# Optimization experiments

Hardware: AMD Instinct MI355X
Metric: run time of the kernel (lower is better)

Reference implementation:

```python
import jax, jax.numpy as jnp
import numpy as np

# UKF constants (Merwe scaled sigma points)
ALPHA, BETA, KAPPA = 1.0, 2.0, 0.0
JITTER = 1e-4
S_DIM, C_DIM, M_DIM, H_DIM = 8, 2, 4, 32


def setup_inputs() -> dict:
    B, T = 1024, 256
    key = jax.random.key(0)
    ks = jax.random.split(key, 11)
    inp = {
        "X0": 0.1 * jax.random.normal(ks[0], (B, S_DIM), dtype=jnp.float32),
        "u": jax.random.normal(ks[1], (B, T, C_DIM), dtype=jnp.float32),
        "y": jax.random.normal(ks[2], (B, T, M_DIM), dtype=jnp.float32),
        # learned process model f(x,u) = x + tanh([x;u] W1 + b1) W2 + b2
        "W1": 0.1 * jax.random.normal(ks[3], (S_DIM + C_DIM, H_DIM), dtype=jnp.float32),
        "b1": jnp.zeros((H_DIM,), dtype=jnp.float32),
        "W2": 0.1 * jax.random.normal(ks[4], (H_DIM, S_DIM), dtype=jnp.float32),
        "b2": jnp.zeros((S_DIM,), dtype=jnp.float32),
        # linear measurement model h(x) = Hm x
        "Hm": 0.3 * jax.random.normal(ks[5], (M_DIM, S_DIM), dtype=jnp.float32),
        # learned diagonal noise / initial covariance (softplus parameterized)
        "lq": -3.0 + 0.1 * jax.random.normal(ks[6], (S_DIM,), dtype=jnp.float32),
        "lr": -2.0 + 0.1 * jax.random.normal(ks[7], (M_DIM,), dtype=jnp.float32),
        "lp0": -1.0 + 0.1 * jax.random.normal(ks[8], (S_DIM,), dtype=jnp.float32),
    }
    return inp


def reference(X0, u, y, W1, b1, W2, b2, Hm, lq, lr, lp0):
    B, n = X0.shape
    T = u.shape[1]
    lam = ALPHA ** 2 * (n + KAPPA) - n
    c = n + lam
    Wm = jnp.concatenate([jnp.array([lam / c], dtype=X0.dtype),
                          jnp.full((2 * n,), 0.5 / c, dtype=X0.dtype)])
    Wc = Wm.at[0].add(1.0 - ALPHA ** 2 + BETA)
    I = jnp.eye(n, dtype=X0.dtype)

    Q = jnp.diag(jax.nn.softplus(lq))            # [n,n] process noise
    R = jnp.diag(jax.nn.softplus(lr))            # [m,m] measurement noise
    P0 = jnp.broadcast_to(jnp.diag(jax.nn.softplus(lp0)), (B, n, n))  # P0(X0)

    def f(pts, u_t):  # pts [B,2n+1,n], u_t [B,C]
        uu = jnp.broadcast_to(u_t[:, None, :], pts.shape[:2] + (u_t.shape[-1],))
        z = jnp.concatenate([pts, uu], axis=-1)
        return pts + jnp.tanh(z @ W1 + b1) @ W2 + b2

    def step(carry, inp_t):
        x, P = carry            # x [B,n], P [B,n,n]
        u_t, y_t = inp_t        # u at i-1, y at i
        # sigma points via Cholesky of scaled covariance
        L = jnp.linalg.cholesky(c * P + JITTER * I)
        offs = jnp.swapaxes(L, -1, -2)  # [B,n,n]: row i = i-th column of L
        pts = jnp.concatenate([x[:, None], x[:, None] + offs, x[:, None] - offs], axis=1)  # [B,2n+1,n]
        # predict
        pts_f = f(pts, u_t)
        x_pred = jnp.einsum('s,bsn->bn', Wm, pts_f)
        dx = pts_f - x_pred[:, None]
        P_pred = jnp.einsum('s,bsn,bsm->bnm', Wc, dx, dx) + Q
        P_pred = 0.5 * (P_pred + jnp.swapaxes(P_pred, -1, -2)) + JITTER * I
        # measurement update (linear h reused on propagated sigma points)
        y_pts = pts_f @ Hm.T
        y_pred = jnp.einsum('s,bsm->bm', Wm, y_pts)
        dy = y_pts - y_pred[:, None]
        Sy = jnp.einsum('s,bsi,bsj->bij', Wc, dy, dy) + R
        Sy = 0.5 * (Sy + jnp.swapaxes(Sy, -1, -2))
        Pxy = jnp.einsum('s,bsn,bsm->bnm', Wc, dx, dy)
        # K = Pxy Sy^{-1} via solve on Sy (SPD)
        K = jnp.swapaxes(jnp.linalg.solve(Sy, jnp.swapaxes(Pxy, -1, -2)), -1, -2)
        x_new = x_pred + jnp.einsum('bnm,bm->bn', K, y_t - y_pred)
        P_new = P_pred - K @ Sy @ jnp.swapaxes(K, -1, -2)
        P_new = 0.5 * (P_new + jnp.swapaxes(P_new, -1, -2)) + JITTER * I
        q_e = 0.5 * jnp.linalg.slogdet(P_pred)[1]  # [B]
        r_e = 0.5 * jnp.linalg.slogdet(Sy)[1]      # [B]
        return (x_new, P_new), (x_new, P_new, q_e, r_e)

    # steps i = 1..T-1 use u[:, i-1] and y[:, i]
    u_seq = jnp.swapaxes(u[:, :T - 1], 0, 1)  # [T-1,B,C]
    y_seq = jnp.swapaxes(y[:, 1:], 0, 1)      # [T-1,B,M]
    _, (Xs, Ps, qs, rs) = jax.lax.scan(step, (X0, P0), (u_seq, y_seq))

    X = jnp.concatenate([X0[:, None], jnp.swapaxes(Xs, 0, 1)], axis=1)        # [B,T,n]
    P = jnp.concatenate([P0[:, None], jnp.swapaxes(Ps, 0, 1)], axis=1)        # [B,T,n,n]
    zcol = jnp.zeros((X0.shape[0], 1), dtype=X0.dtype)
    q_entr = jnp.concatenate([zcol, jnp.swapaxes(qs, 0, 1)], axis=1)          # [B,T]
    r_entr = jnp.concatenate([zcol, jnp.swapaxes(rs, 0, 1)], axis=1)          # [B,T]
    return X, P, q_entr, r_entr
```

## Files before the change

### kernel.cpp

```cpp
#include <hip/hip_runtime.h>
#include <math.h>

#define B_LEN 1024
#define T_LEN 256
#define HST 36
#define TS 20

__device__ __forceinline__ float fast_rcp(float x) { return __builtin_amdgcn_rcpf(x); }
__device__ __forceinline__ float fast_rsq(float x) { return __builtin_amdgcn_rsqf(x); }
__device__ __forceinline__ float lane_bcast(float v, int l) {
    return __int_as_float(__builtin_amdgcn_readlane(__float_as_int(v), l));
}
__device__ __forceinline__ float fast_tanh(float x) {
    float e = __expf(2.0f * x);
    return 1.0f - 2.0f * fast_rcp(e + 1.0f);
}
__device__ __forceinline__ float softplus_f(float x) {
    return (x > 20.0f) ? x : log1pf(expf(x));
}
__device__ __forceinline__ float wdot17(const float* __restrict__ a,
                                        const float* __restrict__ b) {
    float full = 0.0f;
    #pragma unroll
    for (int c = 0; c < 4; ++c) {
        const float4 av = *(const float4*)&a[c * 4];
        const float4 bv = *(const float4*)&b[c * 4];
        full += av.x * bv.x + av.y * bv.y + av.z * bv.z + av.w * bv.w;
    }
    full += a[16] * b[16];
    return 0.0625f * full + 1.9375f * a[0] * b[0];
}

__global__ __launch_bounds__(128, 2)
void ukf_kernel(const float* __restrict__ X0, const float* __restrict__ U,
                const float* __restrict__ Y,  const float* __restrict__ W1,
                const float* __restrict__ B1, const float* __restrict__ W2,
                const float* __restrict__ B2, const float* __restrict__ HM,
                const float* __restrict__ LQ, const float* __restrict__ LR,
                const float* __restrict__ LP0, float* __restrict__ out)
{
    const int tid  = threadIdx.x;
    const int wid  = tid >> 6;
    const int lane = tid & 63;
    const int b    = blockIdx.x;
    const int k8   = lane & 7;
    const int g8   = lane >> 3;
    const int i8   = g8;
    const int j8   = k8;
    const int h32  = lane & 31;
    const int p2   = lane >> 5;
    const int m4   = lane & 3;
    const int sy   = lane >> 2;

    __shared__ __align__(16) float u_sh[T_LEN * 2];
    __shared__ __align__(16) float y_sh[T_LEN * 4];
    __shared__ __align__(16) float pts_sh[17 * 8];
    __shared__ __align__(16) float hid_sh[17 * HST];
    __shared__ __align__(16) float pf_sh[17 * 8];
    __shared__ __align__(16) float dxT_sh[8 * TS];
    __shared__ __align__(16) float ypT_sh[4 * TS];
    __shared__ __align__(16) float xp_sh[8];
    __shared__ __align__(16) float ypred_sh[4];
    __shared__ __align__(16) float Sy_sh[16];
    __shared__ __align__(16) float Si_sh[16];
    __shared__ __align__(16) float Pxy_sh[32];
    __shared__ __align__(16) float K_sh[32];
    __shared__ __align__(16) float Pp_sh[64];

    for (int k = tid; k < T_LEN * 2; k += 128) u_sh[k] = U[(size_t)b * (T_LEN * 2) + k];
    for (int k = tid; k < T_LEN * 4; k += 128) y_sh[k] = Y[(size_t)b * (T_LEN * 4) + k];

    float w1r[10];
    #pragma unroll
    for (int d = 0; d < 10; ++d) w1r[d] = W1[d * 32 + h32];
    const float b1r = B1[h32];
    float w2r[32];
    #pragma unroll
    for (int h = 0; h < 32; ++h) w2r[h] = W2[h * 8 + k8];
    const float b2r = B2[k8];
    float hmr[8];
    #pragma unroll
    for (int d = 0; d < 8; ++d) hmr[d] = HM[m4 * 8 + d];

    const float qdiag = softplus_f(LQ[i8]);
    const float rdiag = softplus_f(LR[m4]);

    const size_t Xbase = (size_t)b * T_LEN * 8;
    const size_t Pbase = (size_t)B_LEN * T_LEN * 8  + (size_t)b * T_LEN * 64;
    const size_t qbase = (size_t)B_LEN * T_LEN * 72 + (size_t)b * T_LEN;
    const size_t rbase = (size_t)B_LEN * T_LEN * 73 + (size_t)b * T_LEN;

    float xn[8], Pc[8];
    {
        const float4 xa = *(const float4*)&X0[b * 8];
        const float4 xb = *(const float4*)&X0[b * 8 + 4];
        xn[0] = xa.x; xn[1] = xa.y; xn[2] = xa.z; xn[3] = xa.w;
        xn[4] = xb.x; xn[5] = xb.y; xn[6] = xb.z; xn[7] = xb.w;
        const float p0k = softplus_f(LP0[k8]);
        #pragma unroll
        for (int i = 0; i < 8; ++i) Pc[i] = (i == k8) ? p0k : 0.0f;
    }
    if (wid == 0) {
        out[Pbase + lane] = Pc[g8];
        if (lane == 0) {
            *(float4*)&out[Xbase]     = make_float4(xn[0], xn[1], xn[2], xn[3]);
            *(float4*)&out[Xbase + 4] = make_float4(xn[4], xn[5], xn[6], xn[7]);
            out[qbase] = 0.0f; out[rbase] = 0.0f;
        }
    }

    for (int t = 1; t < T_LEN; ++t) {
        if (wid == 0) {
            float a[8];
            #pragma unroll
            for (int i = 0; i < 8; ++i) a[i] = 8.0f * Pc[i] + ((i == k8) ? 1e-4f : 0.0f);
            #pragma unroll
            for (int j = 0; j < 8; ++j) {
                const float dj  = lane_bcast(a[j], j);
                const float rv  = fast_rsq(dj);
                const float rv2 = rv * rv;
                float u[8];
                #pragma unroll
                for (int i = j + 1; i < 8; ++i) u[i] = lane_bcast(a[i], j);
                if (k8 == j) {
                    a[j] = dj * rv;
                    #pragma unroll
                    for (int i = j + 1; i < 8; ++i) a[i] *= rv;
                } else if (k8 > j) {
                    const float tt = a[j] * rv2;
                    #pragma unroll
                    for (int i = j + 1; i < 8; ++i) a[i] = fmaf(-tt, u[i], a[i]);
                }
            }
            float Lc[8];
            #pragma unroll
            for (int i = 0; i < 8; ++i) Lc[i] = (i >= k8) ? a[i] : 0.0f;
            if (g8 == 0) {
                *(float4*)&pts_sh[(1 + k8) * 8] =
                    make_float4(xn[0] + Lc[0], xn[1] + Lc[1], xn[2] + Lc[2], xn[3] + Lc[3]);
                *(float4*)&pts_sh[(1 + k8) * 8 + 4] =
                    make_float4(xn[4] + Lc[4], xn[5] + Lc[5], xn[6] + Lc[6], xn[7] + Lc[7]);
            } else if (g8 == 1) {
                *(float4*)&pts_sh[(9 + k8) * 8] =
                    make_float4(xn[0] - Lc[0], xn[1] - Lc[1], xn[2] - Lc[2], xn[3] - Lc[3]);
                *(float4*)&pts_sh[(9 + k8) * 8 + 4] =
                    make_float4(xn[4] - Lc[4], xn[5] - Lc[5], xn[6] - Lc[6], xn[7] - Lc[7]);
            } else if (g8 == 2 && k8 == 0) {
                *(float4*)&pts_sh[0] = make_float4(xn[0], xn[1], xn[2], xn[3]);
                *(float4*)&pts_sh[4] = make_float4(xn[4], xn[5], xn[6], xn[7]);
            }
        }
        __syncthreads();

        {
            const float u0 = u_sh[(t - 1) * 2 + 0];
            const float u1 = u_sh[(t - 1) * 2 + 1];
            const float ub = b1r + u0 * w1r[8] + u1 * w1r[9];
            if (wid == 0) {
                #pragma unroll
                for (int p = 0; p < 4; ++p) {
                    const int s = 2 * p + p2;
                    const float4 pa = *(const float4*)&pts_sh[s * 8];
                    const float4 pb = *(const float4*)&pts_sh[s * 8 + 4];
                    float acc = ub
                        + pa.x * w1r[0] + pa.y * w1r[1] + pa.z * w1r[2] + pa.w * w1r[3]
                        + pb.x * w1r[4] + pb.y * w1r[5] + pb.z * w1r[6] + pb.w * w1r[7];
                    hid_sh[s * HST + h32] = fast_tanh(acc);
                }
            } else {
                #pragma unroll
                for (int p = 0; p < 4; ++p) {
                    const int s = 8 + 2 * p + p2;
                    const float4 pa = *(const float4*)&pts_sh[s * 8];
                    const float4 pb = *(const float4*)&pts_sh[s * 8 + 4];
                    float acc = ub
                        + pa.x * w1r[0] + pa.y * w1r[1] + pa.z * w1r[2] + pa.w * w1r[3]
                        + pb.x * w1r[4] + pb.y * w1r[5] + pb.z * w1r[6] + pb.w * w1r[7];
                    hid_sh[s * HST + h32] = fast_tanh(acc);
                }
                if (p2 == 0) {
                    const float4 pa = *(const float4*)&pts_sh[16 * 8];
                    const float4 pb = *(const float4*)&pts_sh[16 * 8 + 4];
                    float acc = ub
                        + pa.x * w1r[0] + pa.y * w1r[1] + pa.z * w1r[2] + pa.w * w1r[3]
                        + pb.x * w1r[4] + pb.y * w1r[5] + pb.z * w1r[6] + pb.w * w1r[7];
                    hid_sh[16 * HST + h32] = fast_tanh(acc);
                }
            }
            const int srow = (wid == 0) ? g8 : (8 + g8);
            float acc = b2r;
            #pragma unroll
            for (int h = 0; h < 32; h += 4) {
                const float4 hv = *(const float4*)&hid_sh[srow * HST + h];
                acc += hv.x * w2r[h] + hv.y * w2r[h + 1] + hv.z * w2r[h + 2] + hv.w * w2r[h + 3];
            }
            pf_sh[srow * 8 + k8] = pts_sh[srow * 8 + k8] + acc;
            if (wid == 1 && lane < 8) {
                float a16 = b2r;
                #pragma unroll
                for (int h = 0; h < 32; h += 4) {
                    const float4 hv = *(const float4*)&hid_sh[16 * HST + h];
                    a16 += hv.x * w2r[h] + hv.y * w2r[h + 1] + hv.z * w2r[h + 2] + hv.w * w2r[h + 3];
                }
                pf_sh[16 * 8 + lane] = pts_sh[16 * 8 + lane] + a16;
            }
        }
        __syncthreads();

        if (wid == 0) {
            const float v0   = pf_sh[i8 * 8 + j8];
            const float v1   = pf_sh[(8 + i8) * 8 + j8];
            const float pf16 = (i8 == 0) ? pf_sh[16 * 8 + j8] : 0.0f;
            float part = ((i8 == 0) ? pf16 : v0) + v1;
            part += __shfl_xor(part, 8);
            part += __shfl_xor(part, 16);
            part += __shfl_xor(part, 32);
            const float xp = part * 0.0625f;
            if (i8 == 0) xp_sh[j8] = xp;
            dxT_sh[j8 * TS + i8]       = v0 - xp;
            dxT_sh[j8 * TS + 8 + i8]   = v1 - xp;
            if (i8 == 0) dxT_sh[j8 * TS + 16] = pf16 - xp;
        } else {
            float yv0, yv16 = 0.0f;
            {
                const float4 pa = *(const float4*)&pf_sh[sy * 8];
                const float4 pb = *(const float4*)&pf_sh[sy * 8 + 4];
                yv0 = pa.x * hmr[0] + pa.y * hmr[1] + pa.z * hmr[2] + pa.w * hmr[3]
                    + pb.x * hmr[4] + pb.y * hmr[5] + pb.z * hmr[6] + pb.w * hmr[7];
            }
            if (sy == 0) {
                const float4 pa = *(const float4*)&pf_sh[16 * 8];
                const float4 pb = *(const float4*)&pf_sh[16 * 8 + 4];
                yv16 = pa.x * hmr[0] + pa.y * hmr[1] + pa.z * hmr[2] + pa.w * hmr[3]
                     + pb.x * hmr[4] + pb.y * hmr[5] + pb.z * hmr[6] + pb.w * hmr[7];
            }
            float py = (sy == 0) ? yv16 : yv0;
            py += __shfl_xor(py, 4);
            py += __shfl_xor(py, 8);
            py += __shfl_xor(py, 16);
            py += __shfl_xor(py, 32);
            const float ypred = py * 0.0625f;
            if (lane < 4) ypred_sh[lane] = ypred;
            ypT_sh[m4 * TS + sy] = yv0 - ypred;
            if (sy == 0) ypT_sh[m4 * TS + 16] = yv16 - ypred;
        }
        __syncthreads();

        float Ppc[8];
        if (wid == 0) {
            const float Ppred = wdot17(&dxT_sh[i8 * TS], &dxT_sh[j8 * TS])
                              + ((i8 == j8) ? (qdiag + 1e-4f) : 0.0f);
            Pp_sh[lane] = Ppred;
            if (lane < 32) {
                const int ii = lane >> 2, mm = lane & 3;
                Pxy_sh[lane] = wdot17(&dxT_sh[ii * TS], &ypT_sh[mm * TS]);
            }
            #pragma unroll
            for (int i = 0; i < 8; ++i) Ppc[i] = Pp_sh[i * 8 + k8];
        } else {
            if (lane < 16)
                Sy_sh[lane] = wdot17(&ypT_sh[sy * TS], &ypT_sh[m4 * TS])
                            + ((sy == m4) ? rdiag : 0.0f);
            float s_[16];
            {
                const float4 r0v = *(const float4*)&Sy_sh[0];
                const float4 r1v = *(const float4*)&Sy_sh[4];
                const float4 r2v = *(const float4*)&Sy_sh[8];
                const float4 r3v = *(const float4*)&Sy_sh[12];
                s_[0]=r0v.x;  s_[1]=r0v.y;  s_[2]=r0v.z;  s_[3]=r0v.w;
                s_[4]=r1v.x;  s_[5]=r1v.y;  s_[6]=r1v.z;  s_[7]=r1v.w;
                s_[8]=r2v.x;  s_[9]=r2v.y;  s_[10]=r2v.z; s_[11]=r2v.w;
                s_[12]=r3v.x; s_[13]=r3v.y; s_[14]=r3v.z; s_[15]=r3v.w;
            }
            const float d0 = s_[0];
            const float r0 = fast_rsq(d0);
            const float L10 = s_[4] * r0, L20 = s_[8] * r0, L30 = s_[12] * r0;
            const float d1 = s_[5] - L10 * L10;
            const float r1 = fast_rsq(d1);
            const float L21 = (s_[9]  - L20 * L10) * r1;
            const float L31 = (s_[13] - L30 * L10) * r1;
            const float d2_ = s_[10] - L20 * L20 - L21 * L21;
            const float r2 = fast_rsq(d2_);
            const float L32 = (s_[14] - L30 * L20 - L31 * L21) * r2;
            const float d3 = s_[15] - L30 * L30 - L31 * L31 - L32 * L32;
            const float r3 = fast_rsq(d3);
            if (lane == 0)
                out[rbase + t] = 0.5f * (__logf(d0) + __logf(d1) + __logf(d2_) + __logf(d3));
            float z1 = -L10 * r0 * r1;
            float z2 = -(L20 * r0 + L21 * z1) * r2;
            float z3 = -(L30 * r0 + L31 * z1 + L32 * z2) * r3;
            float c03 = z3 * r3;
            float c02 = (z2 - L32 * c03) * r2;
            float c01 = (z1 - L21 * c02 - L31 * c03) * r1;
            float c00 = (r0 - L10 * c01 - L20 * c02 - L30 * c03) * r0;
            float z2b = -L21 * r1 * r2;
            float z3b = -(L31 * r1 + L32 * z2b) * r3;
            float c13 = z3b * r3;
            float c12 = (z2b - L32 * c13) * r2;
            float c11 = (r1 - L21 * c12 - L31 * c13) * r1;
            float c10 = (-L10 * c11 - L20 * c12 - L30 * c13) * r0;
            float z3c = -L32 * r2 * r3;
            float c23 = z3c * r3;
            float c22 = (r2 - L32 * c23) * r2;
            float c21 = (-L21 * c22 - L31 * c23) * r1;
            float c20 = (-L10 * c21 - L20 * c22 - L30 * c23) * r0;
            float c33 = r3 * r3;
            float c32 = (-L32 * c33) * r2;
            float c31 = (-L21 * c32 - L31 * c33) * r1;
            float c30 = (-L10 * c31 - L20 * c32 - L30 * c33) * r0;
            const float s01 = 0.5f * (c01 + c10), s02 = 0.5f * (c02 + c20);
            const float s03 = 0.5f * (c03 + c30), s12 = 0.5f * (c12 + c21);
            const float s13 = 0.5f * (c13 + c31), s23 = 0.5f * (c23 + c32);
            if (lane == 0) {
                *(float4*)&Si_sh[0]  = make_float4(c00, s01, s02, s03);
                *(float4*)&Si_sh[4]  = make_float4(s01, c11, s12, s13);
                *(float4*)&Si_sh[8]  = make_float4(s02, s12, c22, s23);
                *(float4*)&Si_sh[12] = make_float4(s03, s13, s23, c33);
            }
        }
        __syncthreads();

        if (wid == 0) {
            float Si[16];
            {
                const float4 a0 = *(const float4*)&Si_sh[0];
                const float4 a1 = *(const float4*)&Si_sh[4];
                const float4 a2 = *(const float4*)&Si_sh[8];
                const float4 a3 = *(const float4*)&Si_sh[12];
                Si[0]=a0.x;  Si[1]=a0.y;  Si[2]=a0.z;  Si[3]=a0.w;
                Si[4]=a1.x;  Si[5]=a1.y;  Si[6]=a1.z;  Si[7]=a1.w;
                Si[8]=a2.x;  Si[9]=a2.y;  Si[10]=a2.z; Si[11]=a2.w;
                Si[12]=a3.x; Si[13]=a3.y; Si[14]=a3.z; Si[15]=a3.w;
            }
            const float4 pr = *(const float4*)&Pxy_sh[k8 * 4];
            float kk[4];
            #pragma unroll
            for (int aa = 0; aa < 4; ++aa)
                kk[aa] = pr.x * Si[0 * 4 + aa] + pr.y * Si[1 * 4 + aa]
                       + pr.z * Si[2 * 4 + aa] + pr.w * Si[3 * 4 + aa];
            if (g8 == 0) *(float4*)&K_sh[k8 * 4] = make_float4(kk[0], kk[1], kk[2], kk[3]);
            float K_[32];
            #pragma unroll
            for (int r = 0; r < 8; ++r) {
                const float4 kr = *(const float4*)&K_sh[r * 4];
                K_[r * 4 + 0] = kr.x; K_[r * 4 + 1] = kr.y;
                K_[r * 4 + 2] = kr.z; K_[r * 4 + 3] = kr.w;
            }
            #pragma unroll
            for (int i = 0; i < 8; ++i) {
                const float m = K_[i * 4 + 0] * pr.x + K_[i * 4 + 1] * pr.y
                              + K_[i * 4 + 2] * pr.z + K_[i * 4 + 3] * pr.w;
                Pc[i] = Ppc[i] - m + ((i == k8) ? 1e-4f : 0.0f);
            }
            const float4 yt = *(const float4*)&y_sh[t * 4];
            const float4 yp = *(const float4*)&ypred_sh[0];
            const float in0 = yt.x - yp.x, in1 = yt.y - yp.y;
            const float in2 = yt.z - yp.z, in3 = yt.w - yp.w;
            const float4 xpa = *(const float4*)&xp_sh[0];
            const float4 xpb = *(const float4*)&xp_sh[4];
            const float xpv[8] = {xpa.x, xpa.y, xpa.z, xpa.w, xpb.x, xpb.y, xpb.z, xpb.w};
            #pragma unroll
            for (int i = 0; i < 8; ++i)
                xn[i] = xpv[i] + K_[i * 4 + 0] * in0 + K_[i * 4 + 1] * in1
                               + K_[i * 4 + 2] * in2 + K_[i * 4 + 3] * in3;
            out[Pbase + (size_t)t * 64 + lane] = Pc[g8];
            if (lane == 0) {
                *(float4*)&out[Xbase + (size_t)t * 8]     = make_float4(xn[0], xn[1], xn[2], xn[3]);
                *(float4*)&out[Xbase + (size_t)t * 8 + 4] = make_float4(xn[4], xn[5], xn[6], xn[7]);
            }
        } else {
            float aq[8];
            #pragma unroll
            for (int i = 0; i < 8; ++i) aq[i] = Pp_sh[i * 8 + k8];
            float qe = 0.0f;
            #pragma unroll
            for (int j = 0; j < 8; ++j) {
                const float dj  = lane_bcast(aq[j], j);
                qe += 0.5f * __logf(dj);
                const float rv2 = fast_rcp(dj);
                float u[8];
                #pragma unroll
                for (int i = j + 1; i < 8; ++i) u[i] = lane_bcast(aq[i], j);
                if (k8 > j) {
                    const float tt = aq[j] * rv2;
                    #pragma unroll
                    for (int i = j + 1; i < 8; ++i) aq[i] = fmaf(-tt, u[i], aq[i]);
                }
            }
            if (lane == 0) out[qbase + t] = qe;
        }
    }
}

extern "C" void kernel_launch(void* const* d_in, const int* in_sizes, int n_in,
                              void* d_out, int out_size, void* d_ws, size_t ws_size,
                              hipStream_t stream) {
    (void)in_sizes; (void)n_in; (void)out_size; (void)d_ws; (void)ws_size;
    const float* X0 = (const float*)d_in[0];
    const float* U  = (const float*)d_in[1];
    const float* Y  = (const float*)d_in[2];
    const float* W1 = (const float*)d_in[3];
    const float* B1 = (const float*)d_in[4];
    const float* W2 = (const float*)d_in[5];
    const float* B2 = (const float*)d_in[6];
    const float* HM = (const float*)d_in[7];
    const float* LQ = (const float*)d_in[8];
    const float* LR = (const float*)d_in[9];
    const float* LP0 = (const float*)d_in[10];
    float* out = (float*)d_out;
    ukf_kernel<<<dim3(B_LEN), dim3(128), 0, stream>>>(X0, U, Y, W1, B1, W2, B2,
                                                      HM, LQ, LR, LP0, out);
}
```

Before: 933.9 us.

## Collapse UKF kernel to a single wavefront per batch, removing block barriers

Each batch element now runs on one 64-lane wavefront instead of two. That removes every __syncthreads and the Si_sh round-trip through shared memory. The log-determinant Cholesky of P_pred is deferred by one step and interleaved with the sigma-point Cholesky of the next step, and a final pass after the loop handles the last step. The cost is more serial work per wave (all 17 sigma points, plus Sy and Pxy computed together) and half as many threads, traded against barrier latency and better lane utilisation. Correctness now depends on LDS accesses within the wave being ordered without explicit barriers.

```diff
diff --git a/kernel.cpp b/kernel.cpp
--- a/kernel.cpp
+++ b/kernel.cpp
@@ -31,7 +31,7 @@
     return 0.0625f * full + 1.9375f * a[0] * b[0];
 }
 
-__global__ __launch_bounds__(128, 2)
+__global__ __launch_bounds__(64, 1)
 void ukf_kernel(const float* __restrict__ X0, const float* __restrict__ U,
                 const float* __restrict__ Y,  const float* __restrict__ W1,
                 const float* __restrict__ B1, const float* __restrict__ W2,
@@ -39,9 +39,7 @@
                 const float* __restrict__ LQ, const float* __restrict__ LR,
                 const float* __restrict__ LP0, float* __restrict__ out)
 {
-    const int tid  = threadIdx.x;
-    const int wid  = tid >> 6;
-    const int lane = tid & 63;
+    const int lane = threadIdx.x;
     const int b    = blockIdx.x;
     const int k8   = lane & 7;
     const int g8   = lane >> 3;
@@ -62,13 +60,20 @@
     __shared__ __align__(16) float xp_sh[8];
     __shared__ __align__(16) float ypred_sh[4];
     __shared__ __align__(16) float Sy_sh[16];
-    __shared__ __align__(16) float Si_sh[16];
     __shared__ __align__(16) float Pxy_sh[32];
     __shared__ __align__(16) float K_sh[32];
     __shared__ __align__(16) float Pp_sh[64];
 
-    for (int k = tid; k < T_LEN * 2; k += 128) u_sh[k] = U[(size_t)b * (T_LEN * 2) + k];
-    for (int k = tid; k < T_LEN * 4; k += 128) y_sh[k] = Y[(size_t)b * (T_LEN * 4) + k];
+    {
+        const float4* Uv = (const float4*)(U + (size_t)b * (T_LEN * 2));
+        float4* us = (float4*)u_sh;
+        #pragma unroll
+        for (int k = 0; k < 2; ++k) us[k * 64 + lane] = Uv[k * 64 + lane];
+        const float4* Yv = (const float4*)(Y + (size_t)b * (T_LEN * 4));
+        float4* ys = (float4*)y_sh;
+        #pragma unroll
+        for (int k = 0; k < 4; ++k) ys[k * 64 + lane] = Yv[k * 64 + lane];
+    }
 
     float w1r[10];
     #pragma unroll
@@ -82,7 +87,7 @@
     #pragma unroll
     for (int d = 0; d < 8; ++d) hmr[d] = HM[m4 * 8 + d];
 
-    const float qdiag = softplus_f(LQ[i8]);
+    const float qdiag = softplus_f(LQ[g8]);
     const float rdiag = softplus_f(LR[m4]);
 
     const size_t Xbase = (size_t)b * T_LEN * 8;
@@ -90,7 +95,7 @@
     const size_t qbase = (size_t)B_LEN * T_LEN * 72 + (size_t)b * T_LEN;
     const size_t rbase = (size_t)B_LEN * T_LEN * 73 + (size_t)b * T_LEN;
 
-    float xn[8], Pc[8];
+    float xn[8], Pc[8], Ppc[8];
     {
         const float4 xa = *(const float4*)&X0[b * 8];
         const float4 xb = *(const float4*)&X0[b * 8 + 4];
@@ -98,40 +103,49 @@
         xn[4] = xb.x; xn[5] = xb.y; xn[6] = xb.z; xn[7] = xb.w;
         const float p0k = softplus_f(LP0[k8]);
         #pragma unroll
-        for (int i = 0; i < 8; ++i) Pc[i] = (i == k8) ? p0k : 0.0f;
-    }
-    if (wid == 0) {
-        out[Pbase + lane] = Pc[g8];
-        if (lane == 0) {
-            *(float4*)&out[Xbase]     = make_float4(xn[0], xn[1], xn[2], xn[3]);
-            *(float4*)&out[Xbase + 4] = make_float4(xn[4], xn[5], xn[6], xn[7]);
-            out[qbase] = 0.0f; out[rbase] = 0.0f;
-        }
+        for (int i = 0; i < 8; ++i) {
+            Pc[i]  = (i == k8) ? p0k : 0.0f;
+            Ppc[i] = (i == k8) ? 1.0f : 0.0f;
+        }
+    }
+    out[Pbase + lane] = Pc[g8];
+    if (lane == 0) {
+        *(float4*)&out[Xbase]     = make_float4(xn[0], xn[1], xn[2], xn[3]);
+        *(float4*)&out[Xbase + 4] = make_float4(xn[4], xn[5], xn[6], xn[7]);
+        out[rbase] = 0.0f;
     }
 
     for (int t = 1; t < T_LEN; ++t) {
-        if (wid == 0) {
-            float a[8];
-            #pragma unroll
-            for (int i = 0; i < 8; ++i) a[i] = 8.0f * Pc[i] + ((i == k8) ? 1e-4f : 0.0f);
-            #pragma unroll
-            for (int j = 0; j < 8; ++j) {
-                const float dj  = lane_bcast(a[j], j);
-                const float rv  = fast_rsq(dj);
-                const float rv2 = rv * rv;
-                float u[8];
-                #pragma unroll
-                for (int i = j + 1; i < 8; ++i) u[i] = lane_bcast(a[i], j);
-                if (k8 == j) {
-                    a[j] = dj * rv;
-                    #pragma unroll
-                    for (int i = j + 1; i < 8; ++i) a[i] *= rv;
-                } else if (k8 > j) {
-                    const float tt = a[j] * rv2;
-                    #pragma unroll
-                    for (int i = j + 1; i < 8; ++i) a[i] = fmaf(-tt, u[i], a[i]);
-                }
-            }
+        float a[8];
+        #pragma unroll
+        for (int i = 0; i < 8; ++i) a[i] = 8.0f * Pc[i] + ((i == k8) ? 1e-4f : 0.0f);
+        float qe = 0.0f;
+        #pragma unroll
+        for (int j = 0; j < 8; ++j) {
+            const float dj = lane_bcast(a[j], j);
+            const float dq = lane_bcast(Ppc[j], j);
+            const float rv = fast_rsq(dj);
+            const float rq = fast_rcp(dq);
+            qe += __logf(dq);
+            const float sc = (k8 == j) ? rv : 1.0f;
+            const float tc = (k8 > j) ? a[j] * (rv * rv) : 0.0f;
+            const float tq = (k8 > j) ? Ppc[j] * rq : 0.0f;
+            float uc[8], uq[8];
+            #pragma unroll
+            for (int i = j + 1; i < 8; ++i) {
+                uc[i] = lane_bcast(a[i], j);
+                uq[i] = lane_bcast(Ppc[i], j);
+            }
+            #pragma unroll
+            for (int i = j + 1; i < 8; ++i) {
+                a[i]   = sc * a[i] - tc * uc[i];
+                Ppc[i] = fmaf(-tq, uq[i], Ppc[i]);
+            }
+            a[j] = (k8 == j) ? dj * rv : a[j];
+        }
+        if (lane == 0) out[qbase + (t - 1)] = 0.5f * qe;
+
+        {
             float Lc[8];
             #pragma unroll
             for (int i = 0; i < 8; ++i) Lc[i] = (i >= k8) ? a[i] : 0.0f;
@@ -150,44 +164,33 @@
                 *(float4*)&pts_sh[4] = make_float4(xn[4], xn[5], xn[6], xn[7]);
             }
         }
-        __syncthreads();
 
         {
             const float u0 = u_sh[(t - 1) * 2 + 0];
             const float u1 = u_sh[(t - 1) * 2 + 1];
             const float ub = b1r + u0 * w1r[8] + u1 * w1r[9];
-            if (wid == 0) {
-                #pragma unroll
-                for (int p = 0; p < 4; ++p) {
-                    const int s = 2 * p + p2;
-                    const float4 pa = *(const float4*)&pts_sh[s * 8];
-                    const float4 pb = *(const float4*)&pts_sh[s * 8 + 4];
-                    float acc = ub
-                        + pa.x * w1r[0] + pa.y * w1r[1] + pa.z * w1r[2] + pa.w * w1r[3]
-                        + pb.x * w1r[4] + pb.y * w1r[5] + pb.z * w1r[6] + pb.w * w1r[7];
-                    hid_sh[s * HST + h32] = fast_tanh(acc);
-                }
-            } else {
-                #pragma unroll
-                for (int p = 0; p < 4; ++p) {
-                    const int s = 8 + 2 * p + p2;
-                    const float4 pa = *(const float4*)&pts_sh[s * 8];
-                    const float4 pb = *(const float4*)&pts_sh[s * 8 + 4];
-                    float acc = ub
-                        + pa.x * w1r[0] + pa.y * w1r[1] + pa.z * w1r[2] + pa.w * w1r[3]
-                        + pb.x * w1r[4] + pb.y * w1r[5] + pb.z * w1r[6] + pb.w * w1r[7];
-                    hid_sh[s * HST + h32] = fast_tanh(acc);
-                }
-                if (p2 == 0) {
-                    const float4 pa = *(const float4*)&pts_sh[16 * 8];
-                    const float4 pb = *(const float4*)&pts_sh[16 * 8 + 4];
-                    float acc = ub
-                        + pa.x * w1r[0] + pa.y * w1r[1] + pa.z * w1r[2] + pa.w * w1r[3]
-                        + pb.x * w1r[4] + pb.y * w1r[5] + pb.z * w1r[6] + pb.w * w1r[7];
-                    hid_sh[16 * HST + h32] = fast_tanh(acc);
-                }
-            }
-            const int srow = (wid == 0) ? g8 : (8 + g8);
+            #pragma unroll
+            for (int p = 0; p < 8; ++p) {
+                const int s = 2 * p + p2;
+                const float4 pa = *(const float4*)&pts_sh[s * 8];
+                const float4 pb = *(const float4*)&pts_sh[s * 8 + 4];
+                float acc = ub
+                    + pa.x * w1r[0] + pa.y * w1r[1] + pa.z * w1r[2] + pa.w * w1r[3]
+                    + pb.x * w1r[4] + pb.y * w1r[5] + pb.z * w1r[6] + pb.w * w1r[7];
+                hid_sh[s * HST + h32] = fast_tanh(acc);
+            }
+            if (p2 == 0) {
+                const float4 pa = *(const float4*)&pts_sh[16 * 8];
+                const float4 pb = *(const float4*)&pts_sh[16 * 8 + 4];
+                float acc = ub
+                    + pa.x * w1r[0] + pa.y * w1r[1] + pa.z * w1r[2] + pa.w * w1r[3]
+                    + pb.x * w1r[4] + pb.y * w1r[5] + pb.z * w1r[6] + pb.w * w1r[7];
+                hid_sh[16 * HST + h32] = fast_tanh(acc);
+            }
+        }
+        #pragma unroll
+        for (int rr = 0; rr < 2; ++rr) {
+            const int srow = rr * 8 + g8;
             float acc = b2r;
             #pragma unroll
             for (int h = 0; h < 32; h += 4) {
@@ -195,19 +198,18 @@
                 acc += hv.x * w2r[h] + hv.y * w2r[h + 1] + hv.z * w2r[h + 2] + hv.w * w2r[h + 3];
             }
             pf_sh[srow * 8 + k8] = pts_sh[srow * 8 + k8] + acc;
-            if (wid == 1 && lane < 8) {
-                float a16 = b2r;
-                #pragma unroll
-                for (int h = 0; h < 32; h += 4) {
-                    const float4 hv = *(const float4*)&hid_sh[16 * HST + h];
-                    a16 += hv.x * w2r[h] + hv.y * w2r[h + 1] + hv.z * w2r[h + 2] + hv.w * w2r[h + 3];
-                }
-                pf_sh[16 * 8 + lane] = pts_sh[16 * 8 + lane] + a16;
-            }
-        }
-        __syncthreads();
-
-        if (wid == 0) {
+        }
+        if (lane < 8) {
+            float a16 = b2r;
+            #pragma unroll
+            for (int h = 0; h < 32; h += 4) {
+                const float4 hv = *(const float4*)&hid_sh[16 * HST + h];
+                a16 += hv.x * w2r[h] + hv.y * w2r[h + 1] + hv.z * w2r[h + 2] + hv.w * w2r[h + 3];
+            }
+            pf_sh[16 * 8 + lane] = pts_sh[16 * 8 + lane] + a16;
+        }
+
+        {
             const float v0   = pf_sh[i8 * 8 + j8];
             const float v1   = pf_sh[(8 + i8) * 8 + j8];
             const float pf16 = (i8 == 0) ? pf_sh[16 * 8 + j8] : 0.0f;
@@ -217,10 +219,11 @@
             part += __shfl_xor(part, 32);
             const float xp = part * 0.0625f;
             if (i8 == 0) xp_sh[j8] = xp;
-            dxT_sh[j8 * TS + i8]       = v0 - xp;
-            dxT_sh[j8 * TS + 8 + i8]   = v1 - xp;
+            dxT_sh[j8 * TS + i8]     = v0 - xp;
+            dxT_sh[j8 * TS + 8 + i8] = v1 - xp;
             if (i8 == 0) dxT_sh[j8 * TS + 16] = pf16 - xp;
-        } else {
+        }
+        {
             float yv0, yv16 = 0.0f;
             {
                 const float4 pa = *(const float4*)&pf_sh[sy * 8];
@@ -244,94 +247,75 @@
             ypT_sh[m4 * TS + sy] = yv0 - ypred;
             if (sy == 0) ypT_sh[m4 * TS + 16] = yv16 - ypred;
         }
-        __syncthreads();
-
-        float Ppc[8];
-        if (wid == 0) {
-            const float Ppred = wdot17(&dxT_sh[i8 * TS], &dxT_sh[j8 * TS])
-                              + ((i8 == j8) ? (qdiag + 1e-4f) : 0.0f);
-            Pp_sh[lane] = Ppred;
-            if (lane < 32) {
-                const int ii = lane >> 2, mm = lane & 3;
-                Pxy_sh[lane] = wdot17(&dxT_sh[ii * TS], &ypT_sh[mm * TS]);
-            }
+
+        {
+            const float pv = wdot17(&dxT_sh[i8 * TS], &dxT_sh[j8 * TS])
+                           + ((i8 == j8) ? (qdiag + 1e-4f) : 0.0f);
+            Pp_sh[lane] = pv;
+
+            const int r2 = (lane < 32) ? sy : (sy & 3);
+            const float* pa2 = (lane < 32) ? &dxT_sh[r2 * TS] : &ypT_sh[r2 * TS];
+            float v2 = wdot17(pa2, &ypT_sh[m4 * TS]);
+            v2 += ((lane >= 32) && (r2 == m4)) ? rdiag : 0.0f;
+            if (lane < 32)      Pxy_sh[lane] = v2;
+            else if (lane < 48) Sy_sh[r2 * 4 + m4] = v2;
+
             #pragma unroll
             for (int i = 0; i < 8; ++i) Ppc[i] = Pp_sh[i * 8 + k8];
-        } else {
-            if (lane < 16)
-                Sy_sh[lane] = wdot17(&ypT_sh[sy * TS], &ypT_sh[m4 * TS])
-                            + ((sy == m4) ? rdiag : 0.0f);
-            float s_[16];
-            {
-                const float4 r0v = *(const float4*)&Sy_sh[0];
-                const float4 r1v = *(const float4*)&Sy_sh[4];
-                const float4 r2v = *(const float4*)&Sy_sh[8];
-                const float4 r3v = *(const float4*)&Sy_sh[12];
-                s_[0]=r0v.x;  s_[1]=r0v.y;  s_[2]=r0v.z;  s_[3]=r0v.w;
-                s_[4]=r1v.x;  s_[5]=r1v.y;  s_[6]=r1v.z;  s_[7]=r1v.w;
-                s_[8]=r2v.x;  s_[9]=r2v.y;  s_[10]=r2v.z; s_[11]=r2v.w;
-                s_[12]=r3v.x; s_[13]=r3v.y; s_[14]=r3v.z; s_[15]=r3v.w;
-            }
-            const float d0 = s_[0];
+        }
+
+        float Si[16];
+        {
+            const float4 r0v = *(const float4*)&Sy_sh[0];
+            const float4 r1v = *(const float4*)&Sy_sh[4];
+            const float4 r2v = *(const float4*)&Sy_sh[8];
+            const float4 r3v = *(const float4*)&Sy_sh[12];
+            const float d0 = r0v.x;
             const float r0 = fast_rsq(d0);
-            const float L10 = s_[4] * r0, L20 = s_[8] * r0, L30 = s_[12] * r0;
-            const float d1 = s_[5] - L10 * L10;
+            const float L10 = r1v.x * r0, L20 = r2v.x * r0, L30 = r3v.x * r0;
+            const float d1 = r1v.y - L10 * L10;
             const float r1 = fast_rsq(d1);
-            const float L21 = (s_[9]  - L20 * L10) * r1;
-            const float L31 = (s_[13] - L30 * L10) * r1;
-            const float d2_ = s_[10] - L20 * L20 - L21 * L21;
-            const float r2 = fast_rsq(d2_);
-            const float L32 = (s_[14] - L30 * L20 - L31 * L21) * r2;
-            const float d3 = s_[15] - L30 * L30 - L31 * L31 - L32 * L32;
+            const float L21 = (r2v.y - L20 * L10) * r1;
+            const float L31 = (r3v.y - L30 * L10) * r1;
+            const float d2_ = r2v.z - L20 * L20 - L21 * L21;
+            const float rr2 = fast_rsq(d2_);
+            const float L32 = (r3v.z - L30 * L20 - L31 * L21) * rr2;
+            const float d3 = r3v.w - L30 * L30 - L31 * L31 - L32 * L32;
             const float r3 = fast_rsq(d3);
             if (lane == 0)
                 out[rbase + t] = 0.5f * (__logf(d0) + __logf(d1) + __logf(d2_) + __logf(d3));
             float z1 = -L10 * r0 * r1;
-            float z2 = -(L20 * r0 + L21 * z1) * r2;
+            float z2 = -(L20 * r0 + L21 * z1) * rr2;
             float z3 = -(L30 * r0 + L31 * z1 + L32 * z2) * r3;
             float c03 = z3 * r3;
-            float c02 = (z2 - L32 * c03) * r2;
+            float c02 = (z2 - L32 * c03) * rr2;
             float c01 = (z1 - L21 * c02 - L31 * c03) * r1;
             float c00 = (r0 - L10 * c01 - L20 * c02 - L30 * c03) * r0;
-            float z2b = -L21 * r1 * r2;
+            float z2b = -L21 * r1 * rr2;
             float z3b = -(L31 * r1 + L32 * z2b) * r3;
             float c13 = z3b * r3;
-            float c12 = (z2b - L32 * c13) * r2;
+            float c12 = (z2b - L32 * c13) * rr2;
             float c11 = (r1 - L21 * c12 - L31 * c13) * r1;
             float c10 = (-L10 * c11 - L20 * c12 - L30 * c13) * r0;
-            float z3c = -L32 * r2 * r3;
+            float z3c = -L32 * rr2 * r3;
             float c23 = z3c * r3;
-            float c22 = (r2 - L32 * c23) * r2;
+            float c22 = (rr2 - L32 * c23) * rr2;
             float c21 = (-L21 * c22 - L31 * c23) * r1;
             float c20 = (-L10 * c21 - L20 * c22 - L30 * c23) * r0;
             float c33 = r3 * r3;
-            float c32 = (-L32 * c33) * r2;
+            float c32 = (-L32 * c33) * rr2;
             float c31 = (-L21 * c32 - L31 * c33) * r1;
             float c30 = (-L10 * c31 - L20 * c32 - L30 * c33) * r0;
             const float s01 = 0.5f * (c01 + c10), s02 = 0.5f * (c02 + c20);
             const float s03 = 0.5f * (c03 + c30), s12 = 0.5f * (c12 + c21);
             const float s13 = 0.5f * (c13 + c31), s23 = 0.5f * (c23 + c32);
-            if (lane == 0) {
-                *(float4*)&Si_sh[0]  = make_float4(c00, s01, s02, s03);
-                *(float4*)&Si_sh[4]  = make_float4(s01, c11, s12, s13);
-                *(float4*)&Si_sh[8]  = make_float4(s02, s12, c22, s23);
-                *(float4*)&Si_sh[12] = make_float4(s03, s13, s23, c33);
-            }
-        }
-        __syncthreads();
-
-        if (wid == 0) {
-            float Si[16];
-            {
-                const float4 a0 = *(const float4*)&Si_sh[0];
-                const float4 a1 = *(const float4*)&Si_sh[4];
-                const float4 a2 = *(const float4*)&Si_sh[8];
-                const float4 a3 = *(const float4*)&Si_sh[12];
-                Si[0]=a0.x;  Si[1]=a0.y;  Si[2]=a0.z;  Si[3]=a0.w;
-                Si[4]=a1.x;  Si[5]=a1.y;  Si[6]=a1.z;  Si[7]=a1.w;
-                Si[8]=a2.x;  Si[9]=a2.y;  Si[10]=a2.z; Si[11]=a2.w;
-                Si[12]=a3.x; Si[13]=a3.y; Si[14]=a3.z; Si[15]=a3.w;
-            }
+            Si[0]  = c00; Si[1]  = s01; Si[2]  = s02; Si[3]  = s03;
+            Si[4]  = s01; Si[5]  = c11; Si[6]  = s12; Si[7]  = s13;
+            Si[8]  = s02; Si[9]  = s12; Si[10] = c22; Si[11] = s23;
+            Si[12] = s03; Si[13] = s13; Si[14] = s23; Si[15] = c33;
+        }
+
+        {
             const float4 pr = *(const float4*)&Pxy_sh[k8 * 4];
             float kk[4];
             #pragma unroll
@@ -368,27 +352,24 @@
                 *(float4*)&out[Xbase + (size_t)t * 8]     = make_float4(xn[0], xn[1], xn[2], xn[3]);
                 *(float4*)&out[Xbase + (size_t)t * 8 + 4] = make_float4(xn[4], xn[5], xn[6], xn[7]);
             }
-        } else {
-            float aq[8];
-            #pragma unroll
-            for (int i = 0; i < 8; ++i) aq[i] = Pp_sh[i * 8 + k8];
-            float qe = 0.0f;
-            #pragma unroll
-            for (int j = 0; j < 8; ++j) {
-                const float dj  = lane_bcast(aq[j], j);
-                qe += 0.5f * __logf(dj);
-                const float rv2 = fast_rcp(dj);
-                float u[8];
-                #pragma unroll
-                for (int i = j + 1; i < 8; ++i) u[i] = lane_bcast(aq[i], j);
-                if (k8 > j) {
-                    const float tt = aq[j] * rv2;
-                    #pragma unroll
-                    for (int i = j + 1; i < 8; ++i) aq[i] = fmaf(-tt, u[i], aq[i]);
-                }
-            }
-            if (lane == 0) out[qbase + t] = qe;
-        }
+        }
+    }
+
+    {
+        float qe = 0.0f;
+        #pragma unroll
+        for (int j = 0; j < 8; ++j) {
+            const float dq = lane_bcast(Ppc[j], j);
+            const float rq = fast_rcp(dq);
+            qe += __logf(dq);
+            const float tq = (k8 > j) ? Ppc[j] * rq : 0.0f;
+            float uq[8];
+            #pragma unroll
+            for (int i = j + 1; i < 8; ++i) uq[i] = lane_bcast(Ppc[i], j);
+            #pragma unroll
+            for (int i = j + 1; i < 8; ++i) Ppc[i] = fmaf(-tq, uq[i], Ppc[i]);
+        }
+        if (lane == 0) out[qbase + (T_LEN - 1)] = 0.5f * qe;
     }
 }
 
@@ -408,6 +389,6 @@
     const float* LR = (const float*)d_in[9];
     const float* LP0 = (const float*)d_in[10];
     float* out = (float*)d_out;
-    ukf_kernel<<<dim3(B_LEN), dim3(128), 0, stream>>>(X0, U, Y, W1, B1, W2, B2,
-                                                      HM, LQ, LR, LP0, out);
-}
+    ukf_kernel<<<dim3(B_LEN), dim3(64), 0, stream>>>(X0, U, Y, W1, B1, W2, B2,
+                                                     HM, LQ, LR, LP0, out);
+}
```

Result: slower. 1.001 ms (+7.2%).
